# Kernel optimization log

Hardware: AMD Instinct MI355X
Metric: run time of the kernel (lower is better)

The kernel has to match this reference:

```python
import jax, jax.numpy as jnp
import numpy as np

TEMPERATURES = (0.1, 0.5, 1.0)
B, Q, P, N, D = 1024, 128, 32, 128, 64


def _cdist(a, b):
    # Euclidean pairwise distance, matching torch.cdist(p=2): [B,Q,D]x[B,K,D]->[B,Q,K]
    a2 = jnp.sum(a * a, axis=-1, keepdims=True)            # [B,Q,1]
    b2 = jnp.sum(b * b, axis=-1, keepdims=True)            # [B,K,1]
    d2 = a2 + jnp.swapaxes(b2, -1, -2) - 2.0 * jnp.einsum('bqd,bkd->bqk', a, b)
    return jnp.sqrt(jnp.maximum(d2, 0.0))


def _conditioned_V(x, y_pos, y_neg, temperature):
    n_neg = y_neg.shape[1]
    dist_pos = _cdist(x, y_pos)                            # [B,Q,P]
    dist_neg = _cdist(x, y_neg)                            # [B,Q,N]
    dist = jnp.concatenate([dist_neg, dist_pos], axis=-1)  # [B,Q,N+P]
    log_kernel = jnp.maximum(-dist / temperature, -80.0)
    kernel = jnp.exp(log_kernel)
    row_sum = jnp.sum(kernel, axis=-1, keepdims=True)      # [B,Q,1]
    col_sum = jnp.sum(kernel, axis=-2, keepdims=True)      # [B,1,N+P]
    normalizer = jnp.sqrt(jnp.maximum(row_sum * col_sum, 1e-12))
    affinity = kernel / normalizer
    affinity_neg = affinity[:, :, :n_neg]
    affinity_pos = affinity[:, :, n_neg:]
    weight_pos = affinity_pos * jnp.sum(affinity_neg, axis=-1, keepdims=True)
    weight_neg = affinity_neg * jnp.sum(affinity_pos, axis=-1, keepdims=True)
    drift = (jnp.einsum('bqp,bpd->bqd', weight_pos, y_pos)
             - jnp.einsum('bqn,bnd->bqd', weight_neg, y_neg))
    return drift


def setup_inputs() -> dict:
    key = jax.random.key(0)
    kx, kp, kn = jax.random.split(key, 3)
    return {
        'x': jax.random.normal(kx, (B, Q, D), dtype=jnp.float32),
        'y_pos': jax.random.normal(kp, (B, P, D), dtype=jnp.float32),
        'y_neg': jax.random.normal(kn, (B, N, D), dtype=jnp.float32),
    }


def reference(x, y_pos, y_neg):
    # mean cross distance (no grad in original -> stop_gradient)
    mean_dist = jax.lax.stop_gradient(jnp.mean(_cdist(x, y_pos)))
    drift_total = jnp.zeros_like(x)
    for base_t in TEMPERATURES:  # small fixed loop over temperatures, as in source
        adaptive_t = jax.lax.stop_gradient(jnp.maximum(base_t * mean_dist, 1e-6))
        drift_total = drift_total + _conditioned_V(x, y_pos, y_neg, adaptive_t)
    target = jax.lax.stop_gradient(x + drift_total)
    loss = jnp.mean((x - target) ** 2)
    return loss
```

## Files before the change

### kernel.cpp

```cpp
#include <hip/hip_runtime.h>

namespace {
constexpr int B = 1024, Q = 128, P = 32, N = 128, D = 64, K = 160;

__global__ __launch_bounds__(256) void k_meandist(
    const float* __restrict__ x, const float* __restrict__ y_pos,
    double* __restrict__ ws) {
  __shared__ float Yp[P][D];
  __shared__ float ysq[P];
  __shared__ float red[4];
  const int b = blockIdx.x, tid = threadIdx.x;
  const float* yb = y_pos + (size_t)b * P * D;
  for (int i = tid; i < P * D / 4; i += 256)
    reinterpret_cast<float4*>(&Yp[0][0])[i] = reinterpret_cast<const float4*>(yb)[i];
  __syncthreads();
  if (tid < P) {
    float s = 0.f;
    for (int d = 0; d < D; ++d) { float v = Yp[tid][d]; s = fmaf(v, v, s); }
    ysq[tid] = s;
  }
  __syncthreads();
  const int q = tid >> 1, ph = tid & 1;
  const float* xq = x + ((size_t)b * Q + q) * D;
  float acc[16];
#pragma unroll
  for (int j = 0; j < 16; ++j) acc[j] = 0.f;
  float xsq = 0.f;
#pragma unroll 1
  for (int d4 = 0; d4 < 16; ++d4) {
    float4 xv = reinterpret_cast<const float4*>(xq)[d4];
    xsq = fmaf(xv.x, xv.x, fmaf(xv.y, xv.y, fmaf(xv.z, xv.z, fmaf(xv.w, xv.w, xsq))));
#pragma unroll
    for (int j = 0; j < 16; ++j) {
      float4 yv = reinterpret_cast<const float4*>(&Yp[ph * 16 + j][0])[d4];
      acc[j] = fmaf(xv.x, yv.x, fmaf(xv.y, yv.y, fmaf(xv.z, yv.z, fmaf(xv.w, yv.w, acc[j]))));
    }
  }
  float dsum = 0.f;
#pragma unroll
  for (int j = 0; j < 16; ++j) {
    float d2 = xsq + ysq[ph * 16 + j] - 2.f * acc[j];
    dsum += sqrtf(fmaxf(d2, 0.f));
  }
#pragma unroll
  for (int m = 1; m < 64; m <<= 1) dsum += __shfl_xor(dsum, m);
  if ((tid & 63) == 0) red[tid >> 6] = dsum;
  __syncthreads();
  if (tid == 0)
    atomicAdd(ws, (double)(red[0] + red[1] + red[2] + red[3]));
}

__global__
__attribute__((amdgpu_flat_work_group_size(512, 512)))
__attribute__((amdgpu_waves_per_eu(2, 2)))
void k_drift(
    const float* __restrict__ x, const float* __restrict__ y_pos,
    const float* __restrict__ y_neg, double* __restrict__ ws) {
  __shared__ __align__(16) float SM[33296];
  float4* Y4 = (float4*)SM;
  float4* X4 = (float4*)(SM + 10240);
  float*  Cs = SM + 10240;
  float4* C4 = (float4*)(SM + 10240);
  float* rss = SM + 31360;
  float* css = SM + 31744;
  float* uss = SM + 32224;
  float* vss = SM + 32608;
  float* ysq = SM + 32992;
  float* xsq = SM + 33152;
  double* redd = (double*)(SM + 33280);

  const int b = blockIdx.x, tid = threadIdx.x;
  const float4* yn4 = (const float4*)(y_neg + (size_t)b * N * D);
  const float4* yp4 = (const float4*)(y_pos + (size_t)b * P * D);
  const float4* xg  = (const float4*)(x + (size_t)b * Q * D);

  for (int idx = tid; idx < K * 16; idx += 512) {
    int k = idx >> 4, d4 = idx & 15;
    float4 v = (k < N) ? yn4[k * 16 + d4] : yp4[(k - N) * 16 + d4];
    Y4[k * 16 + ((d4 + k) & 15)] = v;
  }
  for (int idx = tid; idx < Q * 16; idx += 512) {
    int q = idx >> 4, d4 = idx & 15;
    X4[q * 16 + ((d4 + (q >> 3)) & 15)] = xg[q * 16 + d4];
  }
  if (tid < 384) { rss[tid] = 0.f; uss[tid] = 0.f; vss[tid] = 0.f; }
  __syncthreads();
  if (tid < K) {
    float s = 0.f;
#pragma unroll
    for (int c = 0; c < 16; ++c) {
      float4 v = Y4[tid * 16 + ((c + tid) & 15)];
      s = fmaf(v.x, v.x, fmaf(v.y, v.y, fmaf(v.z, v.z, fmaf(v.w, v.w, s))));
    }
    ysq[tid] = s;
  }
  if (tid < Q) {
    float s = 0.f;
#pragma unroll
    for (int c = 0; c < 16; ++c) {
      float4 v = X4[tid * 16 + ((c + tid) & 15)];
      s = fmaf(v.x, v.x, fmaf(v.y, v.y, fmaf(v.z, v.z, fmaf(v.w, v.w, s))));
    }
    xsq[tid] = s;
  }
  __syncthreads();

  const int qg = tid & 15, kt = tid >> 4;
  const int qb = qg * 8, kb0 = kt * 5;

  float zz[8][5];
#pragma unroll
  for (int i = 0; i < 8; ++i)
#pragma unroll
    for (int j = 0; j < 5; ++j) zz[i][j] = 0.f;

#pragma unroll 2
  for (int d4 = 0; d4 < 16; ++d4) {
    float4 yv[5];
#pragma unroll
    for (int j = 0; j < 5; ++j) {
      int k = kb0 + j;
      yv[j] = Y4[k * 16 + ((d4 + k) & 15)];
    }
    const int rx = (d4 + qg) & 15;
#pragma unroll
    for (int i = 0; i < 8; ++i) {
      float4 xv = X4[(qb + i) * 16 + rx];
#pragma unroll
      for (int j = 0; j < 5; ++j)
        zz[i][j] = fmaf(xv.x, yv[j].x, fmaf(xv.y, yv[j].y,
                   fmaf(xv.z, yv[j].z, fmaf(xv.w, yv[j].w, zz[i][j]))));
    }
  }

  const float meand = (float)(ws[0] * (1.0 / ((double)B * Q * P)));
  const float invt2 = 1.0f / fmaxf(meand, 1e-6f);
#pragma unroll
  for (int i = 0; i < 8; ++i)
#pragma unroll
    for (int j = 0; j < 5; ++j) {
      float d2 = xsq[qb + i] + ysq[kb0 + j] - 2.f * zz[i][j];
      zz[i][j] = __expf(-sqrtf(fmaxf(d2, 0.f)) * invt2);
    }

#pragma unroll
  for (int t = 0; t < 3; ++t) {
    float ers[8] = {0.f,0.f,0.f,0.f,0.f,0.f,0.f,0.f};
    float ecs[5] = {0.f,0.f,0.f,0.f,0.f};
#pragma unroll
    for (int i = 0; i < 8; ++i)
#pragma unroll
      for (int j = 0; j < 5; ++j) {
        float z = zz[i][j], f;
        if (t == 2) f = z;
        else if (t == 1) f = z * z;
        else { float z2 = z * z, z4 = z2 * z2; f = z4 * z4 * z2; }
        ers[i] += f; ecs[j] += f;
      }
#pragma unroll
    for (int j = 0; j < 5; ++j) {
      float v = ecs[j];
      v += __shfl_xor(v, 1); v += __shfl_xor(v, 2);
      v += __shfl_xor(v, 4); v += __shfl_xor(v, 8);
      if (qg == 0) css[t * 160 + kb0 + j] = v;
    }
#pragma unroll
    for (int i = 0; i < 8; ++i) {
      float v = ers[i];
      v += __shfl_xor(v, 16); v += __shfl_xor(v, 32);
      if ((kt & 3) == 0) atomicAdd(&rss[t * 128 + qb + i], v);
    }
  }
  __syncthreads();
  if (tid < 480) css[tid] = rsqrtf(css[tid]);
  __syncthreads();

#pragma unroll
  for (int t = 0; t < 3; ++t) {
    float icr[5];
#pragma unroll
    for (int j = 0; j < 5; ++j) icr[j] = css[t * 160 + kb0 + j];
    float uu[8] = {0.f,0.f,0.f,0.f,0.f,0.f,0.f,0.f};
    float vv[8] = {0.f,0.f,0.f,0.f,0.f,0.f,0.f,0.f};
#pragma unroll
    for (int i = 0; i < 8; ++i)
#pragma unroll
      for (int j = 0; j < 5; ++j) {
        float z = zz[i][j], f;
        if (t == 2) f = z;
        else if (t == 1) f = z * z;
        else { float z2 = z * z, z4 = z2 * z2; f = z4 * z4 * z2; }
        float a = f * icr[j];
        bool pos = (kb0 + j >= N);
        uu[i] += pos ? a : 0.f;
        vv[i] += pos ? 0.f : a;
      }
#pragma unroll
    for (int i = 0; i < 8; ++i) {
      float u = uu[i];
      u += __shfl_xor(u, 16); u += __shfl_xor(u, 32);
      float v = vv[i];
      v += __shfl_xor(v, 16); v += __shfl_xor(v, 32);
      if ((kt & 3) == 0) {
        atomicAdd(&uss[t * 128 + qb + i], u);
        atomicAdd(&vss[t * 128 + qb + i], v);
      }
    }
  }
  __syncthreads();
  if (tid < 384) {
    float inv = 1.0f / rss[tid];
    uss[tid] *= inv;
    vss[tid] *= inv;
  }
  __syncthreads();

  {
    float ic0[5], ic1[5], ic2[5];
#pragma unroll
    for (int j = 0; j < 5; ++j) {
      ic0[j] = css[0 * 160 + kb0 + j];
      ic1[j] = css[1 * 160 + kb0 + j];
      ic2[j] = css[2 * 160 + kb0 + j];
    }
#pragma unroll
    for (int i = 0; i < 8; ++i) {
      const int q2 = qb + i;
      float u0 = uss[q2], u1 = uss[128 + q2], u2 = uss[256 + q2];
      float v0 = vss[q2], v1 = vss[128 + q2], v2 = vss[256 + q2];
#pragma unroll
      for (int j = 0; j < 5; ++j) {
        const int k = kb0 + j;
        float z = zz[i][j], z2 = z * z, z4 = z2 * z2, z10 = z4 * z4 * z2;
        bool pos = (k >= N);
        float a0 = pos ? v0 : u0, a1 = pos ? v1 : u1, a2 = pos ? v2 : u2;
        float c = fmaf(z, ic2[j] * a2, fmaf(z2, ic1[j] * a1, z10 * (ic0[j] * a0)));
        Cs[k * 132 + q2] = pos ? c : -c;
      }
    }
  }
  __syncthreads();

  const int kc = tid >> 8, qc = (tid >> 3) & 31, dc = tid & 7;
  float dr[4][8];
#pragma unroll
  for (int i = 0; i < 4; ++i)
#pragma unroll
    for (int n = 0; n < 8; ++n) dr[i][n] = 0.f;

#pragma unroll 4
  for (int kk = 0; kk < 80; ++kk) {
    const int k = kc * 80 + kk;
    float4 ca = C4[k * 33 + qc];
    float4 y0 = Y4[k * 16 + ((dc * 2 + k) & 15)];
    float4 y1 = Y4[k * 16 + ((dc * 2 + 1 + k) & 15)];
#define GACC(ii, cv)                               \
    dr[ii][0] = fmaf(cv, y0.x, dr[ii][0]);         \
    dr[ii][1] = fmaf(cv, y0.y, dr[ii][1]);         \
    dr[ii][2] = fmaf(cv, y0.z, dr[ii][2]);         \
    dr[ii][3] = fmaf(cv, y0.w, dr[ii][3]);         \
    dr[ii][4] = fmaf(cv, y1.x, dr[ii][4]);         \
    dr[ii][5] = fmaf(cv, y1.y, dr[ii][5]);         \
    dr[ii][6] = fmaf(cv, y1.z, dr[ii][6]);         \
    dr[ii][7] = fmaf(cv, y1.w, dr[ii][7]);
    GACC(0, ca.x) GACC(1, ca.y) GACC(2, ca.z) GACC(3, ca.w)
#undef GACC
  }
  __syncthreads();

  float4* FB = Y4;
  if (kc == 1) {
#pragma unroll
    for (int i = 0; i < 4; ++i) {
      const int q = qc * 4 + i;
#pragma unroll
      for (int w = 0; w < 2; ++w)
        FB[q * 16 + ((dc * 2 + w + qc) & 15)] =
            make_float4(dr[i][w * 4], dr[i][w * 4 + 1], dr[i][w * 4 + 2], dr[i][w * 4 + 3]);
    }
  }
  __syncthreads();
  if (kc == 0) {
    float tot = 0.f;
#pragma unroll
    for (int i = 0; i < 4; ++i) {
      const int q = qc * 4 + i;
#pragma unroll
      for (int w = 0; w < 2; ++w) {
        float4 v = FB[q * 16 + ((dc * 2 + w + qc) & 15)];
        float a0 = dr[i][w * 4]     + v.x;
        float a1 = dr[i][w * 4 + 1] + v.y;
        float a2 = dr[i][w * 4 + 2] + v.z;
        float a3 = dr[i][w * 4 + 3] + v.w;
        tot = fmaf(a0, a0, tot);
        tot = fmaf(a1, a1, tot);
        tot = fmaf(a2, a2, tot);
        tot = fmaf(a3, a3, tot);
      }
    }
#pragma unroll
    for (int m = 1; m < 64; m <<= 1) tot += __shfl_xor(tot, m);
    if ((tid & 63) == 0) redd[tid >> 6] = (double)tot;
  }
  __syncthreads();
  if (tid == 0)
    atomicAdd(ws + 1, redd[0] + redd[1] + redd[2] + redd[3]);
}

__global__ void k_final(const double* __restrict__ ws, float* __restrict__ out) {
  out[0] = (float)(ws[1] / ((double)B * Q * D));
}

}

extern "C" void kernel_launch(void* const* d_in, const int* in_sizes, int n_in,
                              void* d_out, int out_size, void* d_ws, size_t ws_size,
                              hipStream_t stream) {
  const float* x = (const float*)d_in[0];
  const float* y_pos = (const float*)d_in[1];
  const float* y_neg = (const float*)d_in[2];
  float* out = (float*)d_out;
  double* ws = (double*)d_ws;

  hipMemsetAsync(d_ws, 0, 2 * sizeof(double), stream);
  k_meandist<<<B, 256, 0, stream>>>(x, y_pos, ws);
  k_drift<<<B, 512, 0, stream>>>(x, y_pos, y_neg, ws);
  k_final<<<1, 1, 0, stream>>>(ws, out);
}
```

Before: 229.5 us.

## Split fused drift kernel into coefficient kernel and GEMM kernel via global buffer

Splits the single fused drift kernel into two kernels. The first computes the combined per-temperature weight coefficients for each (k,q) pair and writes them to a global workspace buffer. The second reads those coefficients and runs the weighted sum over Y plus the squared-norm reduction. The split lowers shared memory use per kernel and relaxes waves-per-EU so that occupancy can rise. The cost is an extra ~84 MB round trip of coefficients through global memory and one more launch, and the old fused path is kept as a fallback when the workspace is too small.

```diff
diff --git a/kernel.cpp b/kernel.cpp
--- a/kernel.cpp
+++ b/kernel.cpp
@@ -52,8 +52,278 @@
 
 __global__
 __attribute__((amdgpu_flat_work_group_size(512, 512)))
+__attribute__((amdgpu_waves_per_eu(2, 4)))
+void k_coeff(
+    const float* __restrict__ x, const float* __restrict__ y_pos,
+    const float* __restrict__ y_neg, double* __restrict__ ws,
+    float4* __restrict__ C4g) {
+  __shared__ __align__(16) float SM[16128];
+  float4* Y4  = (float4*)SM;
+  float4* X4c = (float4*)(SM + 10240);
+  float* rss = SM + 14336;
+  float* css = SM + 14720;
+  float* uss = SM + 15200;
+  float* vss = SM + 15584;
+  float* ysq = SM + 15968;
+
+  const int b = blockIdx.x, tid = threadIdx.x;
+  const float4* yn4 = (const float4*)(y_neg + (size_t)b * N * D);
+  const float4* yp4 = (const float4*)(y_pos + (size_t)b * P * D);
+  const float4* xg  = (const float4*)(x + (size_t)b * Q * D);
+
+  for (int idx = tid; idx < K * 16; idx += 512) {
+    int k = idx >> 4, d4 = idx & 15;
+    float4 v = (k < N) ? yn4[k * 16 + d4] : yp4[(k - N) * 16 + d4];
+    Y4[k * 16 + ((d4 + k) & 15)] = v;
+  }
+  if (tid < 384) { rss[tid] = 0.f; uss[tid] = 0.f; vss[tid] = 0.f; }
+  __syncthreads();
+  if (tid < K) {
+    float s = 0.f;
+#pragma unroll
+    for (int c = 0; c < 16; ++c) {
+      float4 v = Y4[tid * 16 + ((c + tid) & 15)];
+      s = fmaf(v.x, v.x, fmaf(v.y, v.y, fmaf(v.z, v.z, fmaf(v.w, v.w, s))));
+    }
+    ysq[tid] = s;
+  }
+
+  const int qg = tid & 15, kt = tid >> 4;
+  const int qb = qg * 8;
+
+  float zz[8][5];
+  float xsq8[8];
+#pragma unroll
+  for (int i = 0; i < 8; ++i) {
+    xsq8[i] = 0.f;
+#pragma unroll
+    for (int j = 0; j < 5; ++j) zz[i][j] = 0.f;
+  }
+
+#pragma unroll 1
+  for (int ch = 0; ch < 2; ++ch) {
+    __syncthreads();
+#pragma unroll
+    for (int r = 0; r < 2; ++r) {
+      int idx = tid + 512 * r;
+      int q = idx >> 3, c = idx & 7;
+      X4c[q * 8 + ((c + (q >> 3)) & 7)] = xg[q * 16 + ch * 8 + c];
+    }
+    __syncthreads();
+#pragma unroll
+    for (int d4 = 0; d4 < 8; ++d4) {
+      const int rx = (d4 + qg) & 7;
+      float4 xv[8];
+#pragma unroll
+      for (int i = 0; i < 8; ++i) xv[i] = X4c[(qb + i) * 8 + rx];
+#pragma unroll
+      for (int i = 0; i < 8; ++i)
+        xsq8[i] = fmaf(xv[i].x, xv[i].x, fmaf(xv[i].y, xv[i].y,
+                  fmaf(xv[i].z, xv[i].z, fmaf(xv[i].w, xv[i].w, xsq8[i]))));
+      const int gd4 = ch * 8 + d4;
+#pragma unroll
+      for (int j = 0; j < 5; ++j) {
+        const int k_ = kt + 32 * j;
+        float4 yv = Y4[k_ * 16 + ((gd4 + k_) & 15)];
+#pragma unroll
+        for (int i = 0; i < 8; ++i)
+          zz[i][j] = fmaf(xv[i].x, yv.x, fmaf(xv[i].y, yv.y,
+                     fmaf(xv[i].z, yv.z, fmaf(xv[i].w, yv.w, zz[i][j]))));
+      }
+    }
+  }
+  const float meand = (float)(ws[0] * (1.0 / ((double)B * Q * P)));
+  const float invt2 = 1.0f / fmaxf(meand, 1e-6f);
+#pragma unroll
+  for (int i = 0; i < 8; ++i)
+#pragma unroll
+    for (int j = 0; j < 5; ++j) {
+      const int k_ = kt + 32 * j;
+      float d2 = xsq8[i] + ysq[k_] - 2.f * zz[i][j];
+      zz[i][j] = __expf(-sqrtf(fmaxf(d2, 0.f)) * invt2);
+    }
+
+#pragma unroll
+  for (int t = 0; t < 3; ++t) {
+    float ers[8] = {0.f,0.f,0.f,0.f,0.f,0.f,0.f,0.f};
+    float ecs[5] = {0.f,0.f,0.f,0.f,0.f};
+#pragma unroll
+    for (int i = 0; i < 8; ++i)
+#pragma unroll
+      for (int j = 0; j < 5; ++j) {
+        float z = zz[i][j], f;
+        if (t == 2) f = z;
+        else if (t == 1) f = z * z;
+        else { float z2 = z * z, z4 = z2 * z2; f = z4 * z4 * z2; }
+        ers[i] += f; ecs[j] += f;
+      }
+#pragma unroll
+    for (int j = 0; j < 5; ++j) {
+      float v = ecs[j];
+      v += __shfl_xor(v, 1); v += __shfl_xor(v, 2);
+      v += __shfl_xor(v, 4); v += __shfl_xor(v, 8);
+      if (qg == 0) css[t * 160 + kt + 32 * j] = v;
+    }
+#pragma unroll
+    for (int i = 0; i < 8; ++i) {
+      float v = ers[i];
+      v += __shfl_xor(v, 16); v += __shfl_xor(v, 32);
+      if ((kt & 3) == 0) atomicAdd(&rss[t * 128 + qb + i], v);
+    }
+  }
+  __syncthreads();
+  if (tid < 480) css[tid] = rsqrtf(css[tid]);
+  __syncthreads();
+
+#pragma unroll
+  for (int t = 0; t < 3; ++t) {
+    float icr[5];
+#pragma unroll
+    for (int j = 0; j < 5; ++j) icr[j] = css[t * 160 + kt + 32 * j];
+    float uu[8] = {0.f,0.f,0.f,0.f,0.f,0.f,0.f,0.f};
+    float vv[8] = {0.f,0.f,0.f,0.f,0.f,0.f,0.f,0.f};
+#pragma unroll
+    for (int i = 0; i < 8; ++i)
+#pragma unroll
+      for (int j = 0; j < 5; ++j) {
+        float z = zz[i][j], f;
+        if (t == 2) f = z;
+        else if (t == 1) f = z * z;
+        else { float z2 = z * z, z4 = z2 * z2; f = z4 * z4 * z2; }
+        float a = f * icr[j];
+        if (j == 4) uu[i] += a; else vv[i] += a;
+      }
+#pragma unroll
+    for (int i = 0; i < 8; ++i) {
+      float u = uu[i];
+      u += __shfl_xor(u, 16); u += __shfl_xor(u, 32);
+      float v = vv[i];
+      v += __shfl_xor(v, 16); v += __shfl_xor(v, 32);
+      if ((kt & 3) == 0) {
+        atomicAdd(&uss[t * 128 + qb + i], u);
+        atomicAdd(&vss[t * 128 + qb + i], v);
+      }
+    }
+  }
+  __syncthreads();
+  if (tid < 384) {
+    float inv = 1.0f / rss[tid];
+    uss[tid] *= inv;
+    vss[tid] *= inv;
+  }
+  __syncthreads();
+
+#pragma unroll
+  for (int j = 0; j < 5; ++j) {
+    const int k_ = kt + 32 * j;
+    const bool pos = (j == 4);
+    const float ic0 = css[k_], ic1 = css[160 + k_], ic2 = css[320 + k_];
+    float c0a[8];
+#pragma unroll
+    for (int i = 0; i < 8; ++i) {
+      const int q2 = qb + i;
+      float a0 = pos ? vss[q2]       : uss[q2];
+      float a1 = pos ? vss[128 + q2] : uss[128 + q2];
+      float a2 = pos ? vss[256 + q2] : uss[256 + q2];
+      float z = zz[i][j], z2 = z * z, z4 = z2 * z2, z10 = z4 * z4 * z2;
+      float c = fmaf(z, ic2 * a2, fmaf(z2, ic1 * a1, z10 * (ic0 * a0)));
+      c0a[i] = pos ? c : -c;
+    }
+    const size_t base = ((size_t)b * K + k_) * 32;
+    C4g[base + 2 * qg]     = make_float4(c0a[0], c0a[1], c0a[2], c0a[3]);
+    C4g[base + 2 * qg + 1] = make_float4(c0a[4], c0a[5], c0a[6], c0a[7]);
+  }
+}
+
+__global__
+__attribute__((amdgpu_flat_work_group_size(512, 512)))
+__attribute__((amdgpu_waves_per_eu(2, 4)))
+void k_gemm(
+    const float* __restrict__ y_pos, const float* __restrict__ y_neg,
+    const float4* __restrict__ C4g, double* __restrict__ ws) {
+  __shared__ __align__(16) float SM[10240];
+  __shared__ double redd[4];
+  float4* Y4 = (float4*)SM;
+
+  const int b = blockIdx.x, tid = threadIdx.x;
+  const float4* yn4 = (const float4*)(y_neg + (size_t)b * N * D);
+  const float4* yp4 = (const float4*)(y_pos + (size_t)b * P * D);
+  for (int idx = tid; idx < K * 16; idx += 512) {
+    int k = idx >> 4, d4 = idx & 15;
+    float4 v = (k < N) ? yn4[k * 16 + d4] : yp4[(k - N) * 16 + d4];
+    Y4[k * 16 + ((d4 + k) & 15)] = v;
+  }
+  __syncthreads();
+
+  const int qc = (tid >> 3) & 31, dc = tid & 7, kc = tid >> 8;
+  float dr[4][8];
+#pragma unroll
+  for (int i = 0; i < 4; ++i)
+#pragma unroll
+    for (int n = 0; n < 8; ++n) dr[i][n] = 0.f;
+
+  const size_t cbase = (size_t)b * K * 32 + qc;
+#pragma unroll 4
+  for (int kk = 0; kk < 80; ++kk) {
+    const int k_ = kc * 80 + kk;
+    float4 cg = C4g[cbase + (size_t)k_ * 32];
+    float4 y0 = Y4[k_ * 16 + ((2 * dc + k_) & 15)];
+    float4 y1 = Y4[k_ * 16 + ((2 * dc + 1 + k_) & 15)];
+#define GACC(ii, cv)                               \
+    dr[ii][0] = fmaf(cv, y0.x, dr[ii][0]);         \
+    dr[ii][1] = fmaf(cv, y0.y, dr[ii][1]);         \
+    dr[ii][2] = fmaf(cv, y0.z, dr[ii][2]);         \
+    dr[ii][3] = fmaf(cv, y0.w, dr[ii][3]);         \
+    dr[ii][4] = fmaf(cv, y1.x, dr[ii][4]);         \
+    dr[ii][5] = fmaf(cv, y1.y, dr[ii][5]);         \
+    dr[ii][6] = fmaf(cv, y1.z, dr[ii][6]);         \
+    dr[ii][7] = fmaf(cv, y1.w, dr[ii][7]);
+    GACC(0, cg.x) GACC(1, cg.y) GACC(2, cg.z) GACC(3, cg.w)
+#undef GACC
+  }
+  __syncthreads();
+
+  float4* FB = Y4;
+  if (kc == 1) {
+#pragma unroll
+    for (int i = 0; i < 4; ++i) {
+      const int q = qc * 4 + i;
+#pragma unroll
+      for (int w = 0; w < 2; ++w)
+        FB[q * 16 + ((2 * dc + w + q) & 15)] =
+            make_float4(dr[i][w*4], dr[i][w*4+1], dr[i][w*4+2], dr[i][w*4+3]);
+    }
+  }
+  __syncthreads();
+  if (kc == 0) {
+    float tot = 0.f;
+#pragma unroll
+    for (int i = 0; i < 4; ++i) {
+      const int q = qc * 4 + i;
+#pragma unroll
+      for (int w = 0; w < 2; ++w) {
+        float4 v = FB[q * 16 + ((2 * dc + w + q) & 15)];
+        float a0 = dr[i][w*4]   + v.x;
+        float a1 = dr[i][w*4+1] + v.y;
+        float a2 = dr[i][w*4+2] + v.z;
+        float a3 = dr[i][w*4+3] + v.w;
+        tot = fmaf(a0, a0, tot); tot = fmaf(a1, a1, tot);
+        tot = fmaf(a2, a2, tot); tot = fmaf(a3, a3, tot);
+      }
+    }
+#pragma unroll
+    for (int m = 1; m < 64; m <<= 1) tot += __shfl_xor(tot, m);
+    if ((tid & 63) == 0) redd[tid >> 6] = (double)tot;
+  }
+  __syncthreads();
+  if (tid == 0)
+    atomicAdd(ws + 1, redd[0] + redd[1] + redd[2] + redd[3]);
+}
+
+__global__
+__attribute__((amdgpu_flat_work_group_size(512, 512)))
 __attribute__((amdgpu_waves_per_eu(2, 2)))
-void k_drift(
+void k_drift_fused(
     const float* __restrict__ x, const float* __restrict__ y_pos,
     const float* __restrict__ y_neg, double* __restrict__ ws) {
   __shared__ __align__(16) float SM[33296];
@@ -276,7 +546,7 @@
 #pragma unroll
       for (int w = 0; w < 2; ++w)
         FB[q * 16 + ((dc * 2 + w + qc) & 15)] =
-            make_float4(dr[i][w * 4], dr[i][w * 4 + 1], dr[i][w * 4 + 2], dr[i][w * 4 + 3]);
+            make_float4(dr[i][w*4], dr[i][w*4+1], dr[i][w*4+2], dr[i][w*4+3]);
     }
   }
   __syncthreads();
@@ -288,14 +558,12 @@
 #pragma unroll
       for (int w = 0; w < 2; ++w) {
         float4 v = FB[q * 16 + ((dc * 2 + w + qc) & 15)];
-        float a0 = dr[i][w * 4]     + v.x;
-        float a1 = dr[i][w * 4 + 1] + v.y;
-        float a2 = dr[i][w * 4 + 2] + v.z;
-        float a3 = dr[i][w * 4 + 3] + v.w;
-        tot = fmaf(a0, a0, tot);
-        tot = fmaf(a1, a1, tot);
-        tot = fmaf(a2, a2, tot);
-        tot = fmaf(a3, a3, tot);
+        float a0 = dr[i][w*4]   + v.x;
+        float a1 = dr[i][w*4+1] + v.y;
+        float a2 = dr[i][w*4+2] + v.z;
+        float a3 = dr[i][w*4+3] + v.w;
+        tot = fmaf(a0, a0, tot); tot = fmaf(a1, a1, tot);
+        tot = fmaf(a2, a2, tot); tot = fmaf(a3, a3, tot);
       }
     }
 #pragma unroll
@@ -322,8 +590,15 @@
   float* out = (float*)d_out;
   double* ws = (double*)d_ws;
 
+  const size_t c_bytes = (size_t)B * K * Q * sizeof(float);
   hipMemsetAsync(d_ws, 0, 2 * sizeof(double), stream);
   k_meandist<<<B, 256, 0, stream>>>(x, y_pos, ws);
-  k_drift<<<B, 512, 0, stream>>>(x, y_pos, y_neg, ws);
+  if (ws_size >= 64 + c_bytes) {
+    float4* C4g = (float4*)((char*)d_ws + 64);
+    k_coeff<<<B, 512, 0, stream>>>(x, y_pos, y_neg, ws, C4g);
+    k_gemm<<<B, 512, 0, stream>>>(y_pos, y_neg, C4g, ws);
+  } else {
+    k_drift_fused<<<B, 512, 0, stream>>>(x, y_pos, y_neg, ws);
+  }
   k_final<<<1, 1, 0, stream>>>(ws, out);
 }
```

After: 405.6 us. +76.7%, slower.

## Double drift kernel block to 1024 threads with chunked X staging

Applied to the files above, without the earlier changes.

The drift kernel now runs with 1024 threads per block. Each thread handles a 4x5 tile of the distance matrix, with k strided by 32, instead of an 8x5 contiguous tile. X is staged through shared memory in two 32-dimension chunks, and the x squared norms are computed inline during the dot-product loop. The final reduction now combines four k-partitions through shared memory instead of two. The goal is more waves per block and fewer registers per thread to hide latency, at the cost of an extra barrier, more atomics and a larger cross-partition reduction.

```diff
diff --git a/kernel.cpp b/kernel.cpp
--- a/kernel.cpp
+++ b/kernel.cpp
@@ -51,38 +51,33 @@
 }
 
 __global__
-__attribute__((amdgpu_flat_work_group_size(512, 512)))
-__attribute__((amdgpu_waves_per_eu(2, 2)))
-void k_drift(
+__attribute__((amdgpu_flat_work_group_size(1024, 1024)))
+__attribute__((amdgpu_waves_per_eu(2, 4)))
+void k_drift3(
     const float* __restrict__ x, const float* __restrict__ y_pos,
     const float* __restrict__ y_neg, double* __restrict__ ws) {
-  __shared__ __align__(16) float SM[33296];
-  float4* Y4 = (float4*)SM;
-  float4* X4 = (float4*)(SM + 10240);
-  float*  Cs = SM + 10240;
-  float4* C4 = (float4*)(SM + 10240);
+  __shared__ __align__(16) float SM[33160];
+  float4* Y4  = (float4*)SM;
+  float4* X4c = (float4*)(SM + 10240);
+  float*  Cs  = SM + 10240;
+  float4* C4  = (float4*)(SM + 10240);
   float* rss = SM + 31360;
   float* css = SM + 31744;
   float* uss = SM + 32224;
   float* vss = SM + 32608;
   float* ysq = SM + 32992;
-  float* xsq = SM + 33152;
-  double* redd = (double*)(SM + 33280);
+  double* redd = (double*)(SM + 33152);
 
   const int b = blockIdx.x, tid = threadIdx.x;
   const float4* yn4 = (const float4*)(y_neg + (size_t)b * N * D);
   const float4* yp4 = (const float4*)(y_pos + (size_t)b * P * D);
   const float4* xg  = (const float4*)(x + (size_t)b * Q * D);
 
-  for (int idx = tid; idx < K * 16; idx += 512) {
+  for (int idx = tid; idx < K * 16; idx += 1024) {
     int k = idx >> 4, d4 = idx & 15;
     float4 v = (k < N) ? yn4[k * 16 + d4] : yp4[(k - N) * 16 + d4];
     Y4[k * 16 + ((d4 + k) & 15)] = v;
   }
-  for (int idx = tid; idx < Q * 16; idx += 512) {
-    int q = idx >> 4, d4 = idx & 15;
-    X4[q * 16 + ((d4 + (q >> 3)) & 15)] = xg[q * 16 + d4];
-  }
   if (tid < 384) { rss[tid] = 0.f; uss[tid] = 0.f; vss[tid] = 0.f; }
   __syncthreads();
   if (tid < K) {
@@ -94,61 +89,66 @@
     }
     ysq[tid] = s;
   }
-  if (tid < Q) {
-    float s = 0.f;
-#pragma unroll
-    for (int c = 0; c < 16; ++c) {
-      float4 v = X4[tid * 16 + ((c + tid) & 15)];
-      s = fmaf(v.x, v.x, fmaf(v.y, v.y, fmaf(v.z, v.z, fmaf(v.w, v.w, s))));
-    }
-    xsq[tid] = s;
-  }
-  __syncthreads();
-
-  const int qg = tid & 15, kt = tid >> 4;
-  const int qb = qg * 8, kb0 = kt * 5;
-
-  float zz[8][5];
-#pragma unroll
-  for (int i = 0; i < 8; ++i)
+
+  const int qg = tid & 31, kt = tid >> 5;
+  const int qb = qg * 4;
+
+  float zz[4][5], xs4[4];
+#pragma unroll
+  for (int i = 0; i < 4; ++i) {
+    xs4[i] = 0.f;
 #pragma unroll
     for (int j = 0; j < 5; ++j) zz[i][j] = 0.f;
-
+  }
+
+#pragma unroll 1
+  for (int ch = 0; ch < 2; ++ch) {
+    if (ch) __syncthreads();
+    {
+      int q = tid >> 3, c = tid & 7;
+      X4c[q * 8 + ((c + (q >> 2)) & 7)] = xg[q * 16 + ch * 8 + c];
+    }
+    __syncthreads();
 #pragma unroll 2
-  for (int d4 = 0; d4 < 16; ++d4) {
-    float4 yv[5];
-#pragma unroll
-    for (int j = 0; j < 5; ++j) {
-      int k = kb0 + j;
-      yv[j] = Y4[k * 16 + ((d4 + k) & 15)];
-    }
-    const int rx = (d4 + qg) & 15;
-#pragma unroll
-    for (int i = 0; i < 8; ++i) {
-      float4 xv = X4[(qb + i) * 16 + rx];
-#pragma unroll
-      for (int j = 0; j < 5; ++j)
-        zz[i][j] = fmaf(xv.x, yv[j].x, fmaf(xv.y, yv[j].y,
-                   fmaf(xv.z, yv[j].z, fmaf(xv.w, yv[j].w, zz[i][j]))));
+    for (int d4 = 0; d4 < 8; ++d4) {
+      const int gd4 = ch * 8 + d4;
+      const int rx = (d4 + qg) & 7;
+      float4 xv[4];
+#pragma unroll
+      for (int i = 0; i < 4; ++i) xv[i] = X4c[(qb + i) * 8 + rx];
+#pragma unroll
+      for (int i = 0; i < 4; ++i)
+        xs4[i] = fmaf(xv[i].x, xv[i].x, fmaf(xv[i].y, xv[i].y,
+                 fmaf(xv[i].z, xv[i].z, fmaf(xv[i].w, xv[i].w, xs4[i]))));
+#pragma unroll
+      for (int j = 0; j < 5; ++j) {
+        const int k_ = kt + 32 * j;
+        float4 yv = Y4[k_ * 16 + ((gd4 + k_) & 15)];
+#pragma unroll
+        for (int i = 0; i < 4; ++i)
+          zz[i][j] = fmaf(xv[i].x, yv.x, fmaf(xv[i].y, yv.y,
+                     fmaf(xv[i].z, yv.z, fmaf(xv[i].w, yv.w, zz[i][j]))));
+      }
     }
   }
 
   const float meand = (float)(ws[0] * (1.0 / ((double)B * Q * P)));
   const float invt2 = 1.0f / fmaxf(meand, 1e-6f);
 #pragma unroll
-  for (int i = 0; i < 8; ++i)
+  for (int i = 0; i < 4; ++i)
 #pragma unroll
     for (int j = 0; j < 5; ++j) {
-      float d2 = xsq[qb + i] + ysq[kb0 + j] - 2.f * zz[i][j];
+      const int k_ = kt + 32 * j;
+      float d2 = xs4[i] + ysq[k_] - 2.f * zz[i][j];
       zz[i][j] = __expf(-sqrtf(fmaxf(d2, 0.f)) * invt2);
     }
 
 #pragma unroll
   for (int t = 0; t < 3; ++t) {
-    float ers[8] = {0.f,0.f,0.f,0.f,0.f,0.f,0.f,0.f};
-    float ecs[5] = {0.f,0.f,0.f,0.f,0.f};
-#pragma unroll
-    for (int i = 0; i < 8; ++i)
+    float ers[4] = {0.f, 0.f, 0.f, 0.f};
+    float ecs[5] = {0.f, 0.f, 0.f, 0.f, 0.f};
+#pragma unroll
+    for (int i = 0; i < 4; ++i)
 #pragma unroll
       for (int j = 0; j < 5; ++j) {
         float z = zz[i][j], f;
@@ -161,14 +161,14 @@
     for (int j = 0; j < 5; ++j) {
       float v = ecs[j];
       v += __shfl_xor(v, 1); v += __shfl_xor(v, 2);
-      v += __shfl_xor(v, 4); v += __shfl_xor(v, 8);
-      if (qg == 0) css[t * 160 + kb0 + j] = v;
-    }
-#pragma unroll
-    for (int i = 0; i < 8; ++i) {
+      v += __shfl_xor(v, 4); v += __shfl_xor(v, 8); v += __shfl_xor(v, 16);
+      if (qg == 0) css[t * 160 + kt + 32 * j] = v;
+    }
+#pragma unroll
+    for (int i = 0; i < 4; ++i) {
       float v = ers[i];
-      v += __shfl_xor(v, 16); v += __shfl_xor(v, 32);
-      if ((kt & 3) == 0) atomicAdd(&rss[t * 128 + qb + i], v);
+      v += __shfl_xor(v, 32);
+      if ((tid & 63) < 32) atomicAdd(&rss[t * 128 + qb + i], v);
     }
   }
   __syncthreads();
@@ -179,11 +179,11 @@
   for (int t = 0; t < 3; ++t) {
     float icr[5];
 #pragma unroll
-    for (int j = 0; j < 5; ++j) icr[j] = css[t * 160 + kb0 + j];
-    float uu[8] = {0.f,0.f,0.f,0.f,0.f,0.f,0.f,0.f};
-    float vv[8] = {0.f,0.f,0.f,0.f,0.f,0.f,0.f,0.f};
-#pragma unroll
-    for (int i = 0; i < 8; ++i)
+    for (int j = 0; j < 5; ++j) icr[j] = css[t * 160 + kt + 32 * j];
+    float uu[4] = {0.f, 0.f, 0.f, 0.f};
+    float vv[4] = {0.f, 0.f, 0.f, 0.f};
+#pragma unroll
+    for (int i = 0; i < 4; ++i)
 #pragma unroll
       for (int j = 0; j < 5; ++j) {
         float z = zz[i][j], f;
@@ -191,17 +191,13 @@
         else if (t == 1) f = z * z;
         else { float z2 = z * z, z4 = z2 * z2; f = z4 * z4 * z2; }
         float a = f * icr[j];
-        bool pos = (kb0 + j >= N);
-        uu[i] += pos ? a : 0.f;
-        vv[i] += pos ? 0.f : a;
-      }
-#pragma unroll
-    for (int i = 0; i < 8; ++i) {
-      float u = uu[i];
-      u += __shfl_xor(u, 16); u += __shfl_xor(u, 32);
-      float v = vv[i];
-      v += __shfl_xor(v, 16); v += __shfl_xor(v, 32);
-      if ((kt & 3) == 0) {
+        if (j == 4) uu[i] += a; else vv[i] += a;
+      }
+#pragma unroll
+    for (int i = 0; i < 4; ++i) {
+      float u = uu[i]; u += __shfl_xor(u, 32);
+      float v = vv[i]; v += __shfl_xor(v, 32);
+      if ((tid & 63) < 32) {
         atomicAdd(&uss[t * 128 + qb + i], u);
         atomicAdd(&vss[t * 128 + qb + i], v);
       }
@@ -216,26 +212,25 @@
   __syncthreads();
 
   {
-    float ic0[5], ic1[5], ic2[5];
+    float ic0a[5], ic1a[5], ic2a[5];
 #pragma unroll
     for (int j = 0; j < 5; ++j) {
-      ic0[j] = css[0 * 160 + kb0 + j];
-      ic1[j] = css[1 * 160 + kb0 + j];
-      ic2[j] = css[2 * 160 + kb0 + j];
-    }
-#pragma unroll
-    for (int i = 0; i < 8; ++i) {
+      const int k_ = kt + 32 * j;
+      ic0a[j] = css[k_]; ic1a[j] = css[160 + k_]; ic2a[j] = css[320 + k_];
+    }
+#pragma unroll
+    for (int i = 0; i < 4; ++i) {
       const int q2 = qb + i;
       float u0 = uss[q2], u1 = uss[128 + q2], u2 = uss[256 + q2];
       float v0 = vss[q2], v1 = vss[128 + q2], v2 = vss[256 + q2];
 #pragma unroll
       for (int j = 0; j < 5; ++j) {
-        const int k = kb0 + j;
+        const int k_ = kt + 32 * j;
+        const bool pos = (j == 4);
+        float a0 = pos ? v0 : u0, a1 = pos ? v1 : u1, a2 = pos ? v2 : u2;
         float z = zz[i][j], z2 = z * z, z4 = z2 * z2, z10 = z4 * z4 * z2;
-        bool pos = (k >= N);
-        float a0 = pos ? v0 : u0, a1 = pos ? v1 : u1, a2 = pos ? v2 : u2;
-        float c = fmaf(z, ic2[j] * a2, fmaf(z2, ic1[j] * a1, z10 * (ic0[j] * a0)));
-        Cs[k * 132 + q2] = pos ? c : -c;
+        float c = fmaf(z, ic2a[j] * a2, fmaf(z2, ic1a[j] * a1, z10 * (ic0a[j] * a0)));
+        Cs[k_ * 132 + q2] = pos ? c : -c;
       }
     }
   }
@@ -249,11 +244,11 @@
     for (int n = 0; n < 8; ++n) dr[i][n] = 0.f;
 
 #pragma unroll 4
-  for (int kk = 0; kk < 80; ++kk) {
-    const int k = kc * 80 + kk;
-    float4 ca = C4[k * 33 + qc];
-    float4 y0 = Y4[k * 16 + ((dc * 2 + k) & 15)];
-    float4 y1 = Y4[k * 16 + ((dc * 2 + 1 + k) & 15)];
+  for (int kk = 0; kk < 40; ++kk) {
+    const int k_ = kc * 40 + kk;
+    float4 ca = C4[k_ * 33 + qc];
+    float4 y0 = Y4[k_ * 16 + ((2 * dc + k_) & 15)];
+    float4 y1 = Y4[k_ * 16 + ((2 * dc + 1 + k_) & 15)];
 #define GACC(ii, cv)                               \
     dr[ii][0] = fmaf(cv, y0.x, dr[ii][0]);         \
     dr[ii][1] = fmaf(cv, y0.y, dr[ii][1]);         \
@@ -269,14 +264,14 @@
   __syncthreads();
 
   float4* FB = Y4;
-  if (kc == 1) {
+  const int c0 = (2 * dc + qc) & 15, c1 = (2 * dc + 1 + qc) & 15;
+  if (kc > 0) {
+    const int off = (kc - 1) * 2048;
 #pragma unroll
     for (int i = 0; i < 4; ++i) {
       const int q = qc * 4 + i;
-#pragma unroll
-      for (int w = 0; w < 2; ++w)
-        FB[q * 16 + ((dc * 2 + w + qc) & 15)] =
-            make_float4(dr[i][w * 4], dr[i][w * 4 + 1], dr[i][w * 4 + 2], dr[i][w * 4 + 3]);
+      FB[off + q * 16 + c0] = make_float4(dr[i][0], dr[i][1], dr[i][2], dr[i][3]);
+      FB[off + q * 16 + c1] = make_float4(dr[i][4], dr[i][5], dr[i][6], dr[i][7]);
     }
   }
   __syncthreads();
@@ -285,18 +280,24 @@
 #pragma unroll
     for (int i = 0; i < 4; ++i) {
       const int q = qc * 4 + i;
-#pragma unroll
-      for (int w = 0; w < 2; ++w) {
-        float4 v = FB[q * 16 + ((dc * 2 + w + qc) & 15)];
-        float a0 = dr[i][w * 4]     + v.x;
-        float a1 = dr[i][w * 4 + 1] + v.y;
-        float a2 = dr[i][w * 4 + 2] + v.z;
-        float a3 = dr[i][w * 4 + 3] + v.w;
-        tot = fmaf(a0, a0, tot);
-        tot = fmaf(a1, a1, tot);
-        tot = fmaf(a2, a2, tot);
-        tot = fmaf(a3, a3, tot);
-      }
+      float4 s0 = FB[q * 16 + c0];
+      float4 t0 = FB[2048 + q * 16 + c0];
+      float4 u0 = FB[4096 + q * 16 + c0];
+      float a0 = dr[i][0] + s0.x + t0.x + u0.x;
+      float a1 = dr[i][1] + s0.y + t0.y + u0.y;
+      float a2 = dr[i][2] + s0.z + t0.z + u0.z;
+      float a3 = dr[i][3] + s0.w + t0.w + u0.w;
+      tot = fmaf(a0, a0, tot); tot = fmaf(a1, a1, tot);
+      tot = fmaf(a2, a2, tot); tot = fmaf(a3, a3, tot);
+      float4 s1 = FB[q * 16 + c1];
+      float4 t1 = FB[2048 + q * 16 + c1];
+      float4 u1 = FB[4096 + q * 16 + c1];
+      float a4 = dr[i][4] + s1.x + t1.x + u1.x;
+      float a5 = dr[i][5] + s1.y + t1.y + u1.y;
+      float a6 = dr[i][6] + s1.z + t1.z + u1.z;
+      float a7 = dr[i][7] + s1.w + t1.w + u1.w;
+      tot = fmaf(a4, a4, tot); tot = fmaf(a5, a5, tot);
+      tot = fmaf(a6, a6, tot); tot = fmaf(a7, a7, tot);
     }
 #pragma unroll
     for (int m = 1; m < 64; m <<= 1) tot += __shfl_xor(tot, m);
@@ -324,6 +325,6 @@
 
   hipMemsetAsync(d_ws, 0, 2 * sizeof(double), stream);
   k_meandist<<<B, 256, 0, stream>>>(x, y_pos, ws);
-  k_drift<<<B, 512, 0, stream>>>(x, y_pos, y_neg, ws);
+  k_drift3<<<B, 1024, 0, stream>>>(x, y_pos, y_neg, ws);
   k_final<<<1, 1, 0, stream>>>(ws, out);
 }
```

Result: slower. 267.6 us (+16.6%).
